# Optimization experiments

Hardware: AMD Instinct MI355X
Metric: run time of the kernel (lower is better)

Reference implementation:

```python
import jax, jax.numpy as jnp
import numpy as np

IN_C = 64
OUT_C = 128
HEADS = 8
DIM = 9 * IN_C  # 576


def unfold3x3_s2(fea):
    # torch.nn.functional.unfold(fea, (3,3), padding=1, stride=2)
    # returns [N, C*9, L] with channel-major (c, kh, kw) ordering.
    N, C, H, W = fea.shape
    Ho, Wo = H // 2, W // 2
    p = jnp.pad(fea, ((0, 0), (0, 0), (1, 1), (1, 1)))
    patches = jnp.stack(
        [p[:, :, ki:ki + 2 * Ho:2, kj:kj + 2 * Wo:2] for ki in range(3) for kj in range(3)],
        axis=2,
    )  # [N, C, 9, Ho, Wo]
    return patches.reshape(N, C * 9, Ho * Wo)


def mhsa(x, w_qkv, b_qkv, w_out, b_out):
    # standard ViT attention: x [B, L, D]
    B, L, D = x.shape
    dh = D // HEADS
    qkv = x @ w_qkv + b_qkv  # [B, L, 3D]
    q, k, v = jnp.split(qkv, 3, axis=-1)
    def heads(t):
        return t.reshape(B, L, HEADS, dh).transpose(0, 2, 1, 3)  # [B, h, L, dh]
    q, k, v = heads(q), heads(k), heads(v)
    scale = dh ** -0.5
    scores = jnp.einsum('bhqd,bhkd->bhqk', q, k) * scale
    attn = jax.nn.softmax(scores, axis=-1)
    o = jnp.einsum('bhqk,bhkd->bhqd', attn, v)  # [B, h, L, dh]
    o = o.transpose(0, 2, 1, 3).reshape(B, L, D)
    return o @ w_out + b_out


def setup_inputs() -> dict:
    key = jax.random.key(0)
    ks = jax.random.split(key, 6)
    s = DIM ** -0.5
    return {
        'fea': jax.random.normal(ks[0], (1, IN_C, 128, 128), dtype=jnp.float32),
        'w_qkv': jax.random.normal(ks[1], (DIM, 3 * DIM), dtype=jnp.float32) * s,
        'b_qkv': jnp.zeros((3 * DIM,), dtype=jnp.float32),
        'w_out': jax.random.normal(ks[2], (DIM, DIM), dtype=jnp.float32) * s,
        'b_out': jnp.zeros((DIM,), dtype=jnp.float32),
        'conv_w': jax.random.normal(ks[3], (OUT_C, IN_C, 3, 3), dtype=jnp.float32) * s,
    }


def reference(fea, w_qkv, b_qkv, w_out, b_out, conv_w):
    N, C, H, W = fea.shape
    Ho, Wo = H // 2, W // 2
    x = unfold3x3_s2(fea).transpose(0, 2, 1)          # [N, L, 9C]
    x = mhsa(x, w_qkv, b_qkv, w_out, b_out) + x       # residual
    # matmul with reshaped conv weights: [N, L, 9C] @ [9C, out_c]
    y = x @ conv_w.reshape(OUT_C, -1).T               # [N, L, out_c]
    y = y.transpose(0, 2, 1).reshape(N, OUT_C, Ho, Wo)  # fold with (1,1) kernel
    return jax.nn.silu(y)
```

## Files before the change

### kernel.cpp

```cpp
#include <hip/hip_runtime.h>
#include <hip/hip_bf16.h>
#include <math.h>

#define L_TOK 4096
#define D_DIM 576
#define NHEADS 8
#define DHEAD 72
#define DPAD 96
#define HSZ ((size_t)NHEADS * L_TOK * DPAD)
#define KSPLIT 4
#define LOG2E 1.4426950408889634f
#define SCALE2 (0.11785113019775792f * 1.4426950408889634f)

typedef __attribute__((ext_vector_type(8))) short short8;
typedef __attribute__((ext_vector_type(4))) short short4v;
typedef __attribute__((ext_vector_type(4))) float float4v;

union F4S8 {
  float4 f4;
  short8 s8;
  __hip_bfloat16 h[8];
};

__device__ inline void tc_body(const float* __restrict__ src,
                               __hip_bfloat16* __restrict__ dst, int R, int C,
                               int bi, int bj, int t, __hip_bfloat16* Ts) {
  const int col = t & 63, row4 = t >> 6;
#pragma unroll
  for (int u = 0; u < 16; u++) {
    int r = u * 4 + row4;
    Ts[r * 68 + col] = __float2bfloat16(src[(size_t)(bj * 64 + r) * C + bi * 64 + col]);
  }
  __syncthreads();
#pragma unroll
  for (int u = 0; u < 16; u++) {
    int c = u * 4 + row4;
    dst[(size_t)(bi * 64 + c) * R + bj * 64 + col] = Ts[col * 68 + c];
  }
}

__global__ __launch_bounds__(256) void prep_all(const float* __restrict__ fea,
                                                const float* __restrict__ w_qkv,
                                                const float* __restrict__ w_out,
                                                const float* __restrict__ conv_w,
                                                __hip_bfloat16* __restrict__ xb,
                                                __hip_bfloat16* __restrict__ WqkvT,
                                                __hip_bfloat16* __restrict__ WoT,
                                                __hip_bfloat16* __restrict__ CwB) {
  __shared__ float Shm[3120];
  const int b = blockIdx.x;
  const int t = threadIdx.x;
  if (b < 512) {
    float* Lf = Shm;
    const int ho = b & 63;
    const int c0 = (b >> 6) * 8;
    for (int e = t; e < 3072; e += 256) {
      int c = e / 384;
      int rr = (e / 128) % 3;
      int w = e & 127;
      int h = 2 * ho + rr - 1;
      float v = 0.f;
      if ((unsigned)h < 128u) v = fea[(size_t)(c0 + c) * 16384 + h * 128 + w];
      Lf[(c * 3 + rr) * 130 + w + 1] = v;
    }
    if (t < 24) { Lf[t * 130] = 0.f; Lf[t * 130 + 129] = 0.f; }
    __syncthreads();
    for (int e = t; e < 576; e += 256) {
      int wo = e / 9, ch = e - wo * 9;
      F4S8 u;
#pragma unroll
      for (int j = 0; j < 8; j++) {
        int dd = ch * 8 + j;
        int c = dd / 9, k = dd - c * 9;
        int ki = k / 3, kj = k - ki * 3;
        u.h[j] = __float2bfloat16(Lf[(c * 3 + ki) * 130 + 2 * wo + kj]);
      }
      *(float4*)(xb + (size_t)(ho * 64 + wo) * D_DIM + c0 * 9 + ch * 8) = u.f4;
    }
  } else if (b < 755) {
    int bb = b - 512;
    tc_body(w_qkv, WqkvT, D_DIM, 1728, bb % 27, bb / 27, t, (__hip_bfloat16*)Shm);
  } else if (b < 836) {
    int bb = b - 755;
    tc_body(w_out, WoT, D_DIM, D_DIM, bb % 9, bb / 9, t, (__hip_bfloat16*)Shm);
  } else {
    int i = (b - 836) * 256 + t;
    CwB[i] = __float2bfloat16(conv_w[i]);
  }
}

template <int EPI, int NMI>
__global__ __launch_bounds__(256) void gemm_mfma(const __hip_bfloat16* __restrict__ A,
                                                 const __hip_bfloat16* __restrict__ Bt,
                                                 const float* __restrict__ bias,
                                                 const __hip_bfloat16* __restrict__ resid,
                                                 __hip_bfloat16* __restrict__ outB,
                                                 __hip_bfloat16* __restrict__ outB2) {
  constexpr int K = D_DIM;
  constexpr int BM = NMI * 32;
  __shared__ __align__(16) __hip_bfloat16 As[BM * 72];
  __shared__ __align__(16) __hip_bfloat16 Bs[64 * 72];
  const int t = threadIdx.x;
  const int wave = t >> 6, lane = t & 63, quad = lane >> 4, l16 = lane & 15;
  const int wm = (wave & 2) * (NMI * 8);
  const int wn = (wave & 1) * 32;
  const int m0 = blockIdx.x * BM, n0 = blockIdx.y * 64;

  float4v acc[NMI][2];
#pragma unroll
  for (int i = 0; i < NMI; i++)
#pragma unroll
    for (int j = 0; j < 2; j++) acc[i][j] = (float4v){0.f, 0.f, 0.f, 0.f};

  const int arow = t >> 3, ach = t & 7;
  for (int k0 = 0; k0 < K; k0 += 64) {
    __syncthreads();
#pragma unroll
    for (int u = 0; u < NMI; u++) {
      int row = u * 32 + arow;
      *(float4*)(&As[row * 72 + ach * 8]) =
          *(const float4*)(A + (size_t)(m0 + row) * K + k0 + ach * 8);
    }
#pragma unroll
    for (int u = 0; u < 2; u++) {
      int row = u * 32 + arow;
      *(float4*)(&Bs[row * 72 + ach * 8]) =
          *(const float4*)(Bt + (size_t)(n0 + row) * K + k0 + ach * 8);
    }
    __syncthreads();
    short8 af[NMI][2], bfr[2][2];
#pragma unroll
    for (int i = 0; i < NMI; i++)
#pragma unroll
      for (int s = 0; s < 2; s++)
        af[i][s] = *(const short8*)(&As[(wm + i * 16 + l16) * 72 + s * 32 + quad * 8]);
#pragma unroll
    for (int j = 0; j < 2; j++)
#pragma unroll
      for (int s = 0; s < 2; s++)
        bfr[j][s] = *(const short8*)(&Bs[(wn + j * 16 + l16) * 72 + s * 32 + quad * 8]);
#pragma unroll
    for (int i = 0; i < NMI; i++)
#pragma unroll
      for (int j = 0; j < 2; j++) {
        acc[i][j] = __builtin_amdgcn_mfma_f32_16x16x32_bf16(af[i][0], bfr[j][0], acc[i][j], 0, 0, 0);
        acc[i][j] = __builtin_amdgcn_mfma_f32_16x16x32_bf16(af[i][1], bfr[j][1], acc[i][j], 0, 0, 0);
      }
  }

  if (EPI == 0) {
    const int part = n0 / D_DIM;
    if (part < 2) {
      __hip_bfloat16* dst = outB + (size_t)part * HSZ;
      const float sc = (part == 0) ? SCALE2 : 1.f;
#pragma unroll
      for (int j = 0; j < 2; j++) {
        int ng = n0 + wn + j * 16 + l16;
        float bv = bias[ng];
        int rem = ng - part * D_DIM;
        int h = rem / DHEAD;
        int d = rem - h * DHEAD;
#pragma unroll
        for (int i = 0; i < NMI; i++) {
          int mb = m0 + wm + i * 16 + quad * 4;
#pragma unroll
          for (int r = 0; r < 4; r++)
            dst[((size_t)h * L_TOK + mb + r) * DPAD + d] =
                __float2bfloat16((acc[i][j][r] + bv) * sc);
        }
      }
    } else {
      __hip_bfloat16* Ls = As;
      __syncthreads();
      const int n0rel = n0 - 2 * D_DIM;
#pragma unroll
      for (int j = 0; j < 2; j++) {
        int nloc = wn + j * 16 + l16;
        float bv = bias[n0 + nloc];
#pragma unroll
        for (int i = 0; i < NMI; i++) {
          int mloc = wm + i * 16 + quad * 4;
#pragma unroll
          for (int r = 0; r < 4; r++)
            Ls[nloc * 136 + mloc + r] = __float2bfloat16(acc[i][j][r] + bv);
        }
      }
      __syncthreads();
      for (int e = t; e < 1024; e += 256) {
        int row = e >> 4, ch = e & 15;
        int ng = n0rel + row;
        int hh = ng / DHEAD, dd = ng - hh * DHEAD;
        *(float4*)(outB2 + ((size_t)hh * DPAD + dd) * L_TOK + m0 + ch * 8) =
            *(const float4*)(&Ls[row * 136 + ch * 8]);
      }
    }
  } else {
#pragma unroll
    for (int j = 0; j < 2; j++) {
      int ng = n0 + wn + j * 16 + l16;
      float bv = bias[ng];
#pragma unroll
      for (int i = 0; i < NMI; i++) {
        int mb = m0 + wm + i * 16 + quad * 4;
#pragma unroll
        for (int r = 0; r < 4; r++) {
          size_t idx = (size_t)(mb + r) * D_DIM + ng;
          float v = acc[i][j][r] + bv + __bfloat162float(resid[idx]);
          outB[idx] = __float2bfloat16(v);
        }
      }
    }
  }
}

__global__ __launch_bounds__(256) void final_small(const __hip_bfloat16* __restrict__ A,
                                                   const __hip_bfloat16* __restrict__ Bt,
                                                   float* __restrict__ out) {
  __shared__ __align__(16) __hip_bfloat16 As[32 * 72];
  __shared__ __align__(16) __hip_bfloat16 Bs[32 * 72];
  const int t = threadIdx.x;
  const int wave = t >> 6, lane = t & 63, quad = lane >> 4, l16 = lane & 15;
  const int wm = (wave & 2) * 8;
  const int wn = (wave & 1) * 16;
  const int m0 = blockIdx.x * 32, n0 = blockIdx.y * 32;

  float4v acc = (float4v){0.f, 0.f, 0.f, 0.f};

  const int arow = t >> 3, ach = t & 7;
  for (int k0 = 0; k0 < D_DIM; k0 += 64) {
    __syncthreads();
    *(float4*)(&As[arow * 72 + ach * 8]) =
        *(const float4*)(A + (size_t)(m0 + arow) * D_DIM + k0 + ach * 8);
    *(float4*)(&Bs[arow * 72 + ach * 8]) =
        *(const float4*)(Bt + (size_t)(n0 + arow) * D_DIM + k0 + ach * 8);
    __syncthreads();
    short8 af[2], bfr[2];
#pragma unroll
    for (int s = 0; s < 2; s++) {
      af[s] = *(const short8*)(&As[(wm + l16) * 72 + s * 32 + quad * 8]);
      bfr[s] = *(const short8*)(&Bs[(wn + l16) * 72 + s * 32 + quad * 8]);
    }
    acc = __builtin_amdgcn_mfma_f32_16x16x32_bf16(af[0], bfr[0], acc, 0, 0, 0);
    acc = __builtin_amdgcn_mfma_f32_16x16x32_bf16(af[1], bfr[1], acc, 0, 0, 0);
  }
  const int oc = n0 + wn + l16;
  const int mb = m0 + wm + quad * 4;
#pragma unroll
  for (int r = 0; r < 4; r++) {
    float v = acc[r];
    float sg = 1.f / (1.f + __expf(-v));
    out[(size_t)oc * L_TOK + mb + r] = v * sg;
  }
}

#define KS_STRIDE 104
#define VT_STRIDE 72
#define PS_STRIDE 40
#define KBUF (64 * KS_STRIDE)
#define VBUF (80 * VT_STRIDE)

__global__ __launch_bounds__(256, 2) void attn_mfma(const __hip_bfloat16* __restrict__ Qb,
                                                    const __hip_bfloat16* __restrict__ Kb,
                                                    const __hip_bfloat16* __restrict__ VbT,
                                                    __hip_bfloat16* __restrict__ Opart,
                                                    float* __restrict__ Ml) {
  __shared__ __align__(16) __hip_bfloat16 Ks[2 * KBUF];
  __shared__ __align__(16) __hip_bfloat16 Vt[2 * VBUF];
  __shared__ __align__(16) __hip_bfloat16 Ps[4 * 64 * PS_STRIDE];

  const int bid = blockIdx.x;
  const int h = bid & 7;
  const int rest = bid >> 3;
  const int ksp = rest & 3;
  const int qblk = rest >> 2;
  const int t = threadIdx.x;
  const int wave = t >> 6;
  const int lane = t & 63;
  const int quad = lane >> 4;
  const int l16 = lane & 15;

  const __hip_bfloat16* Qh = Qb + (size_t)h * L_TOK * DPAD;
  const __hip_bfloat16* Kh = Kb + (size_t)h * L_TOK * DPAD;
  const __hip_bfloat16* VhT = VbT + (size_t)h * DPAD * L_TOK;

  const int qbase = qblk * 256 + wave * 64;
  short8 qf[4][3];
#pragma unroll
  for (int mi = 0; mi < 4; mi++) {
#pragma unroll
    for (int s = 0; s < 3; s++) {
      if (s == 2 && quad >= 1) {
        qf[mi][s] = (short8){0, 0, 0, 0, 0, 0, 0, 0};
        if (quad == 1) qf[mi][s][0] = (short)0xC100;
      } else {
        qf[mi][s] = *(const short8*)(Qh + (size_t)(qbase + mi * 16 + l16) * DPAD + s * 32 + quad * 8);
      }
    }
  }

  const float4 zero4 = {0.f, 0.f, 0.f, 0.f};
  union { float4 f4; unsigned u[4]; } kpad, vones;
  kpad.u[0] = 0x00003F80u; kpad.u[1] = 0u; kpad.u[2] = 0u; kpad.u[3] = 0u;
  vones.u[0] = vones.u[1] = vones.u[2] = vones.u[3] = 0x3F803F80u;
  if (t < 192) {
    int row = t / 3, ch = 9 + t % 3;
    float4 kv = (ch == 9) ? kpad.f4 : zero4;
    *(float4*)(&Ks[row * KS_STRIDE + ch * 8]) = kv;
    *(float4*)(&Ks[KBUF + row * KS_STRIDE + ch * 8]) = kv;
  } else {
    int e = t - 192;
    int d = 72 + (e >> 3), ch = e & 7;
    float4 vv = (d == 72) ? vones.f4 : zero4;
    *(float4*)(&Vt[d * VT_STRIDE + ch * 8]) = vv;
    *(float4*)(&Vt[VBUF + d * VT_STRIDE + ch * 8]) = vv;
  }

  float4v Of[4][5];
#pragma unroll
  for (int mi = 0; mi < 4; mi++)
#pragma unroll
    for (int nt = 0; nt < 5; nt++) Of[mi][nt] = (float4v){0.f, 0.f, 0.f, 0.f};

  __hip_bfloat16* myPs = Ps + wave * 64 * PS_STRIDE;
  const int kstart = ksp * 1024;

  auto stage = [&](int kbase, __hip_bfloat16* Kw, __hip_bfloat16* Vw) {
    for (int e = t; e < 576; e += 256) {
      int row = e / 9, ch = e - row * 9;
      *(float4*)(&Kw[row * KS_STRIDE + ch * 8]) =
          *(const float4*)(Kh + (size_t)(kbase + row) * DPAD + ch * 8);
    }
    for (int e = t; e < 576; e += 256) {
      int d = e >> 3, ch = e & 7;
      *(float4*)(&Vw[d * VT_STRIDE + ch * 8]) =
          *(const float4*)(VhT + (size_t)d * L_TOK + kbase + ch * 8);
    }
  };

  stage(kstart, Ks, Vt);
  __syncthreads();

  for (int kt = 0; kt < 16; kt++) {
    const int p = kt & 1;
    if (kt + 1 < 16)
      stage(kstart + (kt + 1) * 64, Ks + (1 - p) * KBUF, Vt + (1 - p) * VBUF);

    const __hip_bfloat16* Ksb = Ks + p * KBUF;
    const __hip_bfloat16* Vtb = Vt + p * VBUF;

    float4v S[4][4];
#pragma unroll
    for (int ks = 0; ks < 4; ks++) {
      float4v a0 = (float4v){0.f, 0.f, 0.f, 0.f};
      float4v a1 = a0, a2 = a0, a3 = a0;
#pragma unroll
      for (int s = 0; s < 3; s++) {
        short8 kf = *(const short8*)(&Ksb[(ks * 16 + l16) * KS_STRIDE + s * 32 + quad * 8]);
        a0 = __builtin_amdgcn_mfma_f32_16x16x32_bf16(kf, qf[0][s], a0, 0, 0, 0);
        a1 = __builtin_amdgcn_mfma_f32_16x16x32_bf16(kf, qf[1][s], a1, 0, 0, 0);
        a2 = __builtin_amdgcn_mfma_f32_16x16x32_bf16(kf, qf[2][s], a2, 0, 0, 0);
        a3 = __builtin_amdgcn_mfma_f32_16x16x32_bf16(kf, qf[3][s], a3, 0, 0, 0);
      }
#pragma unroll
      for (int r = 0; r < 4; r++) {
        S[0][ks][r] = a0[r]; S[1][ks][r] = a1[r];
        S[2][ks][r] = a2[r]; S[3][ks][r] = a3[r];
      }
    }

#pragma unroll
    for (int kstep = 0; kstep < 2; kstep++) {
#pragma unroll
      for (int mi = 0; mi < 4; mi++) {
#pragma unroll
        for (int k2 = 0; k2 < 2; k2++) {
          int ks = kstep * 2 + k2;
          union { short4v v; __hip_bfloat16 hh[4]; } pk;
#pragma unroll
          for (int r = 0; r < 4; r++) {
            float pr = exp2f(S[mi][ks][r]);
            pk.hh[r] = __float2bfloat16(pr);
          }
          *(short4v*)(&myPs[(mi * 16 + l16) * PS_STRIDE + k2 * 16 + quad * 4]) = pk.v;
        }
      }
      short8 pa[4];
#pragma unroll
      for (int mi = 0; mi < 4; mi++)
        pa[mi] = *(const short8*)(&myPs[(mi * 16 + l16) * PS_STRIDE + quad * 8]);
#pragma unroll
      for (int nt = 0; nt < 5; nt++) {
        short8 vb = *(const short8*)(&Vtb[(nt * 16 + l16) * VT_STRIDE + kstep * 32 + quad * 8]);
        Of[0][nt] = __builtin_amdgcn_mfma_f32_16x16x32_bf16(pa[0], vb, Of[0][nt], 0, 0, 0);
        Of[1][nt] = __builtin_amdgcn_mfma_f32_16x16x32_bf16(pa[1], vb, Of[1][nt], 0, 0, 0);
        Of[2][nt] = __builtin_amdgcn_mfma_f32_16x16x32_bf16(pa[2], vb, Of[2][nt], 0, 0, 0);
        Of[3][nt] = __builtin_amdgcn_mfma_f32_16x16x32_bf16(pa[3], vb, Of[3][nt], 0, 0, 0);
      }
    }

    __syncthreads();
  }

  const size_t pb = ((size_t)ksp * NHEADS + h) * L_TOK;
#pragma unroll
  for (int mi = 0; mi < 4; mi++) {
#pragma unroll
    for (int nt = 0; nt < 5; nt++) {
      int d = nt * 16 + l16;
      if (d < DHEAD) {
#pragma unroll
        for (int r = 0; r < 4; r++) {
          int q = qbase + mi * 16 + quad * 4 + r;
          Opart[(pb + q) * 72 + d] = __float2bfloat16(Of[mi][nt][r]);
        }
      }
    }
  }
  if (l16 == 8) {
#pragma unroll
    for (int mi = 0; mi < 4; mi++) {
#pragma unroll
      for (int r = 0; r < 4; r++)
        Ml[pb + qbase + mi * 16 + quad * 4 + r] = Of[mi][4][r];
    }
  }
}

__global__ __launch_bounds__(256) void attn_merge(const __hip_bfloat16* __restrict__ Opart,
                                                  const float* __restrict__ Ml,
                                                  __hip_bfloat16* __restrict__ ob) {
  int idx = blockIdx.x * 256 + threadIdx.x;
  int h = idx / (L_TOK * 9);
  int rem = idx - h * (L_TOK * 9);
  int q = rem / 9;
  int ch = rem - q * 9;
  float denom = 0.f;
  float acc[8] = {0, 0, 0, 0, 0, 0, 0, 0};
#pragma unroll
  for (int s = 0; s < KSPLIT; s++) {
    size_t b = ((size_t)s * NHEADS + h) * L_TOK + q;
    denom += Ml[b];
    short8 o = *(const short8*)(Opart + b * 72 + ch * 8);
#pragma unroll
    for (int j = 0; j < 8; j++) {
      union { short ss; __hip_bfloat16 bb; } u;
      u.ss = o[j];
      acc[j] += __bfloat162float(u.bb);
    }
  }
  float inv = 1.f / denom;
  __hip_bfloat16* dst = ob + (size_t)q * D_DIM + h * DHEAD + ch * 8;
#pragma unroll
  for (int j = 0; j < 8; j++) dst[j] = __float2bfloat16(acc[j] * inv);
}

extern "C" void kernel_launch(void* const* d_in, const int* in_sizes, int n_in,
                              void* d_out, int out_size, void* d_ws, size_t ws_size,
                              hipStream_t stream) {
  const float* fea    = (const float*)d_in[0];
  const float* w_qkv  = (const float*)d_in[1];
  const float* b_qkv  = (const float*)d_in[2];
  const float* w_out  = (const float*)d_in[3];
  const float* b_out  = (const float*)d_in[4];
  const float* conv_w = (const float*)d_in[5];
  float* out = (float*)d_out;

  __hip_bfloat16* xb    = (__hip_bfloat16*)d_ws;
  __hip_bfloat16* WqkvT = xb + (size_t)L_TOK * D_DIM;
  __hip_bfloat16* WoT   = WqkvT + (size_t)1728 * D_DIM;
  __hip_bfloat16* CwB   = WoT + (size_t)D_DIM * D_DIM;
  __hip_bfloat16* QKb   = CwB + (size_t)128 * D_DIM;
  __hip_bfloat16* VbT   = QKb + 2 * HSZ;
  __hip_bfloat16* Opart = VbT + HSZ;
  float* Ml = (float*)(Opart + (size_t)KSPLIT * NHEADS * L_TOK * 72);
  __hip_bfloat16* ob = QKb;
  __hip_bfloat16* xr = Opart;

  prep_all<<<1124, 256, 0, stream>>>(fea, w_qkv, w_out, conv_w, xb, WqkvT, WoT, CwB);
  gemm_mfma<0, 4><<<dim3(32, 27), 256, 0, stream>>>(xb, WqkvT, b_qkv, nullptr, QKb, VbT);
  attn_mfma<<<512, 256, 0, stream>>>(QKb, QKb + HSZ, VbT, Opart, Ml);
  attn_merge<<<1152, 256, 0, stream>>>(Opart, Ml, ob);
  gemm_mfma<1, 2><<<dim3(64, 9), 256, 0, stream>>>(ob, WoT, b_out, xb, xr, nullptr);
  final_small<<<dim3(128, 4), 256, 0, stream>>>(xr, CwB, out);
}
```

Before: 181.5 us.

## Replace LDS round-trip for P fragments with permlane swaps and add MFMA priority hints

The softmax probability tile was written to per-wave shared memory and read back in the MFMA A-operand layout. It is now packed into bf16 pairs in registers and redistributed across lanes with permlane32_swap/permlane16_swap, which removes the LDS stores, loads and shared buffer. s_setprio is also raised around the two MFMA phases so waves doing matrix work get issue priority. This adds register pressure for the packed P values and depends on the lane permutation matching the fragment layout exactly.

```diff
diff --git a/kernel.cpp b/kernel.cpp
--- a/kernel.cpp
+++ b/kernel.cpp
@@ -15,6 +15,7 @@
 typedef __attribute__((ext_vector_type(8))) short short8;
 typedef __attribute__((ext_vector_type(4))) short short4v;
 typedef __attribute__((ext_vector_type(4))) float float4v;
+typedef __attribute__((ext_vector_type(2))) int int2v;
 
 union F4S8 {
   float4 f4;
@@ -255,7 +256,6 @@
 
 #define KS_STRIDE 104
 #define VT_STRIDE 72
-#define PS_STRIDE 40
 #define KBUF (64 * KS_STRIDE)
 #define VBUF (80 * VT_STRIDE)
 
@@ -266,7 +266,6 @@
                                                     float* __restrict__ Ml) {
   __shared__ __align__(16) __hip_bfloat16 Ks[2 * KBUF];
   __shared__ __align__(16) __hip_bfloat16 Vt[2 * VBUF];
-  __shared__ __align__(16) __hip_bfloat16 Ps[4 * 64 * PS_STRIDE];
 
   const int bid = blockIdx.x;
   const int h = bid & 7;
@@ -321,7 +320,6 @@
 #pragma unroll
     for (int nt = 0; nt < 5; nt++) Of[mi][nt] = (float4v){0.f, 0.f, 0.f, 0.f};
 
-  __hip_bfloat16* myPs = Ps + wave * 64 * PS_STRIDE;
   const int kstart = ksp * 1024;
 
   auto stage = [&](int kbase, __hip_bfloat16* Kw, __hip_bfloat16* Vw) {
@@ -349,6 +347,7 @@
     const __hip_bfloat16* Vtb = Vt + p * VBUF;
 
     float4v S[4][4];
+    __builtin_amdgcn_s_setprio(1);
 #pragma unroll
     for (int ks = 0; ks < 4; ks++) {
       float4v a0 = (float4v){0.f, 0.f, 0.f, 0.f};
@@ -367,27 +366,35 @@
         S[2][ks][r] = a2[r]; S[3][ks][r] = a3[r];
       }
     }
+    __builtin_amdgcn_s_setprio(0);
+
+    int pk[4][4][2];
+#pragma unroll
+    for (int mi = 0; mi < 4; mi++)
+#pragma unroll
+      for (int ks = 0; ks < 4; ks++)
+#pragma unroll
+        for (int rp = 0; rp < 2; rp++) {
+          union { int u; __hip_bfloat16 hh[2]; } pu;
+          pu.hh[0] = __float2bfloat16(exp2f(S[mi][ks][2 * rp]));
+          pu.hh[1] = __float2bfloat16(exp2f(S[mi][ks][2 * rp + 1]));
+          pk[mi][ks][rp] = pu.u;
+        }
 
 #pragma unroll
     for (int kstep = 0; kstep < 2; kstep++) {
+      short8 pa[4];
 #pragma unroll
       for (int mi = 0; mi < 4; mi++) {
-#pragma unroll
-        for (int k2 = 0; k2 < 2; k2++) {
-          int ks = kstep * 2 + k2;
-          union { short4v v; __hip_bfloat16 hh[4]; } pk;
-#pragma unroll
-          for (int r = 0; r < 4; r++) {
-            float pr = exp2f(S[mi][ks][r]);
-            pk.hh[r] = __float2bfloat16(pr);
-          }
-          *(short4v*)(&myPs[(mi * 16 + l16) * PS_STRIDE + k2 * 16 + quad * 4]) = pk.v;
-        }
-      }
-      short8 pa[4];
-#pragma unroll
-      for (int mi = 0; mi < 4; mi++)
-        pa[mi] = *(const short8*)(&myPs[(mi * 16 + l16) * PS_STRIDE + quad * 8]);
+        int2v t0 = __builtin_amdgcn_permlane32_swap(pk[mi][2 * kstep][0], pk[mi][2 * kstep + 1][0], false, false);
+        int2v u0 = __builtin_amdgcn_permlane16_swap(t0[0], t0[1], false, false);
+        int2v t1 = __builtin_amdgcn_permlane32_swap(pk[mi][2 * kstep][1], pk[mi][2 * kstep + 1][1], false, false);
+        int2v u1 = __builtin_amdgcn_permlane16_swap(t1[0], t1[1], false, false);
+        union { int u[4]; short8 s; } pb_;
+        pb_.u[0] = u0[0]; pb_.u[1] = u1[0]; pb_.u[2] = u0[1]; pb_.u[3] = u1[1];
+        pa[mi] = pb_.s;
+      }
+      __builtin_amdgcn_s_setprio(1);
 #pragma unroll
       for (int nt = 0; nt < 5; nt++) {
         short8 vb = *(const short8*)(&Vtb[(nt * 16 + l16) * VT_STRIDE + kstep * 32 + quad * 8]);
@@ -396,6 +403,7 @@
         Of[2][nt] = __builtin_amdgcn_mfma_f32_16x16x32_bf16(pa[2], vb, Of[2][nt], 0, 0, 0);
         Of[3][nt] = __builtin_amdgcn_mfma_f32_16x16x32_bf16(pa[3], vb, Of[3][nt], 0, 0, 0);
       }
+      __builtin_amdgcn_s_setprio(0);
     }
 
     __syncthreads();
```

Result: slower. 188.6 us (+4.0%).

## Prefetch K/V tiles into registers and defer LDS writes past compute

Applied to the files above, without the earlier changes.

The attention inner loop now issues the global loads for the next K/V tile into registers at the start of each iteration and writes them to shared memory only after the MFMA work, so load latency overlaps compute instead of stalling before it. Address offsets are precomputed once, and the loop is unrolled by two so the double-buffer pointers are compile-time. s_setprio brackets around the MFMA sections raise wave priority during matrix math. The cost is extra register pressure from six float4 staging registers, plus one redundant load on the final iteration.

```diff
diff --git a/kernel.cpp b/kernel.cpp
--- a/kernel.cpp
+++ b/kernel.cpp
@@ -324,31 +324,51 @@
   __hip_bfloat16* myPs = Ps + wave * 64 * PS_STRIDE;
   const int kstart = ksp * 1024;
 
-  auto stage = [&](int kbase, __hip_bfloat16* Kw, __hip_bfloat16* Vw) {
-    for (int e = t; e < 576; e += 256) {
-      int row = e / 9, ch = e - row * 9;
-      *(float4*)(&Kw[row * KS_STRIDE + ch * 8]) =
-          *(const float4*)(Kh + (size_t)(kbase + row) * DPAD + ch * 8);
-    }
-    for (int e = t; e < 576; e += 256) {
-      int d = e >> 3, ch = e & 7;
-      *(float4*)(&Vw[d * VT_STRIDE + ch * 8]) =
-          *(const float4*)(VhT + (size_t)d * L_TOK + kbase + ch * 8);
+  int kgo[3], klo[3], vgo[3], vlo[3];
+#pragma unroll
+  for (int u = 0; u < 3; u++) {
+    int e = t + u * 256;
+    int ee = (e < 576) ? e : 0;
+    int row = ee / 9, ch = ee - row * 9;
+    kgo[u] = row * (DPAD * 2) + ch * 16;
+    klo[u] = row * (KS_STRIDE * 2) + ch * 16;
+    int d = ee >> 3, c2 = ee & 7;
+    vgo[u] = d * (L_TOK * 2) + c2 * 16;
+    vlo[u] = d * (VT_STRIDE * 2) + c2 * 16;
+  }
+  const bool has3 = (t < 64);
+
+  float4 krg0, krg1, krg2, vrg0, vrg1, vrg2;
+  auto stage_load = [&](int kbase) {
+    const char* Kt_ = (const char*)(Kh + (size_t)kbase * DPAD);
+    const char* Vg_ = (const char*)(VhT + kbase);
+    krg0 = *(const float4*)(Kt_ + kgo[0]);
+    krg1 = *(const float4*)(Kt_ + kgo[1]);
+    vrg0 = *(const float4*)(Vg_ + vgo[0]);
+    vrg1 = *(const float4*)(Vg_ + vgo[1]);
+    if (has3) {
+      krg2 = *(const float4*)(Kt_ + kgo[2]);
+      vrg2 = *(const float4*)(Vg_ + vgo[2]);
     }
   };
-
-  stage(kstart, Ks, Vt);
-  __syncthreads();
-
-  for (int kt = 0; kt < 16; kt++) {
-    const int p = kt & 1;
-    if (kt + 1 < 16)
-      stage(kstart + (kt + 1) * 64, Ks + (1 - p) * KBUF, Vt + (1 - p) * VBUF);
-
-    const __hip_bfloat16* Ksb = Ks + p * KBUF;
-    const __hip_bfloat16* Vtb = Vt + p * VBUF;
+  auto stage_write = [&](__hip_bfloat16* Kw, __hip_bfloat16* Vw) {
+    *(float4*)((char*)Kw + klo[0]) = krg0;
+    *(float4*)((char*)Kw + klo[1]) = krg1;
+    *(float4*)((char*)Vw + vlo[0]) = vrg0;
+    *(float4*)((char*)Vw + vlo[1]) = vrg1;
+    if (has3) {
+      *(float4*)((char*)Kw + klo[2]) = krg2;
+      *(float4*)((char*)Vw + vlo[2]) = vrg2;
+    }
+  };
+
+  auto body = [&](int kt, const __hip_bfloat16* Ksb, const __hip_bfloat16* Vtb,
+                  __hip_bfloat16* Kw, __hip_bfloat16* Vw) {
+    const int knext = (kt < 15) ? kt + 1 : 15;
+    stage_load(kstart + knext * 64);
 
     float4v S[4][4];
+    __builtin_amdgcn_s_setprio(1);
 #pragma unroll
     for (int ks = 0; ks < 4; ks++) {
       float4v a0 = (float4v){0.f, 0.f, 0.f, 0.f};
@@ -367,6 +387,7 @@
         S[2][ks][r] = a2[r]; S[3][ks][r] = a3[r];
       }
     }
+    __builtin_amdgcn_s_setprio(0);
 
 #pragma unroll
     for (int kstep = 0; kstep < 2; kstep++) {
@@ -377,10 +398,8 @@
           int ks = kstep * 2 + k2;
           union { short4v v; __hip_bfloat16 hh[4]; } pk;
 #pragma unroll
-          for (int r = 0; r < 4; r++) {
-            float pr = exp2f(S[mi][ks][r]);
-            pk.hh[r] = __float2bfloat16(pr);
-          }
+          for (int r = 0; r < 4; r++)
+            pk.hh[r] = __float2bfloat16(exp2f(S[mi][ks][r]));
           *(short4v*)(&myPs[(mi * 16 + l16) * PS_STRIDE + k2 * 16 + quad * 4]) = pk.v;
         }
       }
@@ -388,6 +407,7 @@
 #pragma unroll
       for (int mi = 0; mi < 4; mi++)
         pa[mi] = *(const short8*)(&myPs[(mi * 16 + l16) * PS_STRIDE + quad * 8]);
+      __builtin_amdgcn_s_setprio(1);
 #pragma unroll
       for (int nt = 0; nt < 5; nt++) {
         short8 vb = *(const short8*)(&Vtb[(nt * 16 + l16) * VT_STRIDE + kstep * 32 + quad * 8]);
@@ -396,9 +416,20 @@
         Of[2][nt] = __builtin_amdgcn_mfma_f32_16x16x32_bf16(pa[2], vb, Of[2][nt], 0, 0, 0);
         Of[3][nt] = __builtin_amdgcn_mfma_f32_16x16x32_bf16(pa[3], vb, Of[3][nt], 0, 0, 0);
       }
-    }
-
+      __builtin_amdgcn_s_setprio(0);
+    }
+
+    stage_write(Kw, Vw);
     __syncthreads();
+  };
+
+  stage_load(kstart);
+  stage_write(Ks, Vt);
+  __syncthreads();
+
+  for (int kt2 = 0; kt2 < 16; kt2 += 2) {
+    body(kt2,     Ks,        Vt,        Ks + KBUF, Vt + VBUF);
+    body(kt2 + 1, Ks + KBUF, Vt + VBUF, Ks,        Vt);
   }
 
   const size_t pb = ((size_t)ksp * NHEADS + h) * L_TOK;
```

Result: no change. 178.6 us (-1.6%).
